# Kernel optimization log

Measured on AMD Instinct MI355X. Metric: run time of the kernel, lower is better.

Reference implementation:

```python
import jax, jax.numpy as jnp
import numpy as np

N_EMBD = 768
N_HEAD = 12
HEAD_DIM = N_EMBD // N_HEAD  # 64


def setup_inputs() -> dict:
    key = jax.random.key(0)
    k1, k2, k3 = jax.random.split(key, 3)
    B, S = 4, 2048
    x = jax.random.normal(k1, (B, S, N_EMBD), dtype=jnp.float32)
    W_attn = jax.random.normal(k2, (N_EMBD, 3 * N_EMBD), dtype=jnp.float32) * 0.02
    b_attn = jax.random.normal(k3, (3 * N_EMBD,), dtype=jnp.float32) * 0.02
    return {"x": x, "W_attn": W_attn, "b_attn": b_attn}


def reference(x, W_attn, b_attn):
    B, S, E = x.shape
    H, D = N_HEAD, HEAD_DIM
    # fused QKV projection (torch Linear: x @ W^T + b; here W_attn stored as [E, 3E])
    qkv = x @ W_attn + b_attn  # [B, S, 3E]
    q, k, v = jnp.split(qkv, 3, axis=-1)
    q = q.reshape(B, S, H, D)
    k = k.reshape(B, S, H, D)
    v = v.reshape(B, S, H, D)
    scale = 1.0 / np.sqrt(D).astype(np.float32)
    scores = jnp.einsum('bqhd,bkhd->bhqk', q, k) * scale  # [B, H, S, S]
    causal = jnp.tril(jnp.ones((S, S), dtype=bool))
    # ReLU attention nonlinearity (no softmax); masked entries -> 0
    att = jnp.where(causal, jnp.maximum(scores, 0.0), 0.0)
    y = jnp.einsum('bhqk,bkhd->bqhd', att, v)  # [B, S, H, D]
    return y.reshape(B, S, E)
```

## Files before the change

### kernel.cpp

```cpp
#include <hip/hip_runtime.h>

typedef __attribute__((ext_vector_type(8))) short short8;
typedef __attribute__((ext_vector_type(4))) float floatx4;
typedef __attribute__((ext_vector_type(4))) unsigned int uint4v;

#define S_LEN 2048
#define NH 12
#define HD 64
#define EMB 768
#define E3 2304

__device__ __forceinline__ unsigned short f2bf(float f) {
    unsigned int u = __builtin_bit_cast(unsigned int, f);
    u += 0x7FFFu + ((u >> 16) & 1u);
    return (unsigned short)(u >> 16);
}

__device__ __forceinline__ unsigned int pack2bf(float a, float b) {
#if __has_builtin(__builtin_amdgcn_cvt_pk_bf16_f32)
    typedef __attribute__((ext_vector_type(2))) short short2v;
    short2v r = __builtin_amdgcn_cvt_pk_bf16_f32(a, b);
    return __builtin_bit_cast(unsigned int, r);
#else
    return (unsigned int)f2bf(a) | ((unsigned int)f2bf(b) << 16);
#endif
}

__device__ __forceinline__ void pl32_swap(unsigned int& x, unsigned int& y) {
#if __has_builtin(__builtin_amdgcn_permlane32_swap)
    typedef __attribute__((ext_vector_type(2))) unsigned int uint2v_;
    uint2v_ r = __builtin_amdgcn_permlane32_swap(x, y, false, false);
    x = r[0]; y = r[1];
#else
    asm("v_permlane32_swap_b32 %0, %1" : "+v"(x), "+v"(y));
#endif
}
__device__ __forceinline__ void pl16_swap(unsigned int& x, unsigned int& y) {
#if __has_builtin(__builtin_amdgcn_permlane16_swap)
    typedef __attribute__((ext_vector_type(2))) unsigned int uint2v_;
    uint2v_ r = __builtin_amdgcn_permlane16_swap(x, y, false, false);
    x = r[0]; y = r[1];
#else
    asm("v_permlane16_swap_b32 %0, %1" : "+v"(x), "+v"(y));
#endif
}

__device__ __forceinline__ void gl_lds16(const void* g, void* l) {
    __builtin_amdgcn_global_load_lds(
        (const __attribute__((address_space(1))) unsigned int*)g,
        (__attribute__((address_space(3))) unsigned int*)l, 16, 0, 0);
}

__global__ __launch_bounds__(256) void conv_fused(const float* __restrict__ x,
                                                  ushort* __restrict__ xb,
                                                  const float* __restrict__ W,
                                                  ushort* __restrict__ Wt) {
    int tid = threadIdx.x;
    if (blockIdx.x < 6144) {
        int i = (blockIdx.x * 256 + tid) * 4;
        float4 f = *(const float4*)(x + i);
        ushort4 o;
        o.x = f2bf(f.x); o.y = f2bf(f.y); o.z = f2bf(f.z); o.w = f2bf(f.w);
        *(ushort4*)(xb + i) = o;
    } else {
        __shared__ float tile[32][33];
        int b2 = blockIdx.x - 6144;
        int n0 = (b2 % 72) * 32, k0 = (b2 / 72) * 32;
        int tx = tid & 31, ty = tid >> 5;
        for (int i = 0; i < 4; i++)
            tile[ty + i * 8][tx] = W[(size_t)(k0 + ty + i * 8) * E3 + n0 + tx];
        __syncthreads();
        for (int i = 0; i < 4; i++)
            Wt[(size_t)(n0 + ty + i * 8) * EMB + k0 + tx] = f2bf(tile[tx][ty + i * 8]);
    }
}

__global__ __launch_bounds__(256) void qkv_gemm(const ushort* __restrict__ Xb,
                                                const ushort* __restrict__ Wt,
                                                const float* __restrict__ bias,
                                                ushort* __restrict__ QKb,
                                                ushort* __restrict__ Vt) {
    __shared__ ushort lds[16896];
    char* ldsb = (char*)lds;
    int tid  = threadIdx.x;
    int wv = tid >> 6, lane = tid & 63;
    int l15 = lane & 15, quad = lane >> 4;
    int r8 = lane >> 3, cc = lane & 7;
    int wm = wv >> 1, wn = wv & 1;
    int m0 = blockIdx.x * 128, n0 = blockIdx.y * 128;

    floatx4 acc[4][4] = {};

    const char* ag = (const char*)(Xb + (size_t)m0 * EMB)
                   + (wv * 32 + r8) * 1536 + (cc ^ r8) * 16;
    const char* bgp = (const char*)(Wt + (size_t)n0 * EMB)
                   + (wv * 32 + r8) * 1536 + (cc ^ r8) * 16;
    int ast = (wv * 32) * 128;
    int bst = 16384 + (wv * 32) * 128;
    int afo[2], bfo[2];
    for (int ch = 0; ch < 2; ch++) {
        int sw = ((ch * 4 + quad) ^ (l15 & 7)) * 16;
        afo[ch] = wm * 8192 + l15 * 128 + sw;
        bfo[ch] = 16384 + wn * 8192 + l15 * 128 + sw;
    }

    for (int k0 = 0; k0 < 12; k0++) {
        __syncthreads();
        for (int i = 0; i < 4; i++) {
            gl_lds16(ag + i * 12288, ldsb + ast + i * 1024);
            gl_lds16(bgp + i * 12288, ldsb + bst + i * 1024);
        }
        ag += 128;  bgp += 128;
        __syncthreads();
        for (int ch = 0; ch < 2; ch++) {
            short8 af[4], bf[4];
            for (int mi = 0; mi < 4; mi++)
                af[mi] = *(const short8*)(ldsb + afo[ch] + mi * 2048);
            for (int ni = 0; ni < 4; ni++)
                bf[ni] = *(const short8*)(ldsb + bfo[ch] + ni * 2048);
            for (int mi = 0; mi < 4; mi++)
                for (int ni = 0; ni < 4; ni++)
                    acc[mi][ni] = __builtin_amdgcn_mfma_f32_16x16x32_bf16(
                        af[mi], bf[ni], acc[mi][ni], 0, 0, 0);
        }
    }

    __syncthreads();
    int seg = n0 / EMB;
    if (seg < 2) {
        float scale = (seg == 0) ? 0.125f : 1.0f;
        for (int ni = 0; ni < 4; ni++) {
            int nl = wn * 64 + ni * 16 + l15;
            float bv = bias[n0 + nl];
            for (int mi = 0; mi < 4; mi++)
                for (int r = 0; r < 4; r++) {
                    int ml = wm * 64 + mi * 16 + quad * 4 + r;
                    lds[ml * 132 + nl] = f2bf((acc[mi][ni][r] + bv) * scale);
                }
        }
        __syncthreads();
        int row = tid >> 1, half2 = tid & 1;
        size_t gm = (size_t)(m0 + row);
        for (int i = 0; i < 8; i++) {
            uint4 v = *(const uint4*)&lds[row * 132 + half2 * 64 + i * 8];
            *(uint4*)&QKb[gm * 1536 + n0 + half2 * 64 + i * 8] = v;
        }
    } else {
        for (int ni = 0; ni < 4; ni++) {
            int nl = wn * 64 + ni * 16 + l15;
            float bv = bias[n0 + nl];
            for (int mi = 0; mi < 4; mi++) {
                int ml = wm * 64 + mi * 16 + quad * 4;
                ushort4 p4;
                p4.x = f2bf(acc[mi][ni][0] + bv);
                p4.y = f2bf(acc[mi][ni][1] + bv);
                p4.z = f2bf(acc[mi][ni][2] + bv);
                p4.w = f2bf(acc[mi][ni][3] + bv);
                *(ushort4*)&lds[nl * 132 + ml] = p4;
            }
        }
        __syncthreads();
        int row = tid >> 1, half2 = tid & 1;
        int nn = n0 + row - 1536;
        int hh = nn >> 6, d = nn & 63;
        int bb = m0 >> 11, s0 = m0 & 2047;
        for (int i = 0; i < 8; i++) {
            uint4 v = *(const uint4*)&lds[row * 132 + half2 * 64 + i * 8];
            *(uint4*)&Vt[((size_t)(bb * NH + hh) * HD + d) * S_LEN + s0 + half2 * 64 + i * 8] = v;
        }
    }
}

__global__ __launch_bounds__(256) void attn(const ushort* __restrict__ QKb,
                                            const ushort* __restrict__ Vt,
                                            float* __restrict__ out) {
    __shared__ ushort lds[32768];
    char* ldsb = (char*)lds;
    int tid = threadIdx.x;
    int w = tid >> 6, lane = tid & 63;
    int l15 = lane & 15, quad = lane >> 4;
    int r8 = lane >> 3, cc = lane & 7;
    int rr = lane >> 4;

    int kfo[2];
    for (int ch = 0; ch < 2; ch++)
        kfo[ch] = l15 * 128 + ((ch * 4 + quad) ^ (l15 & 7)) * 16;
    int vfo2[4];
    for (int T = 0; T < 4; T++)
        vfo2[T] = 32768 + l15 * 256 + ((T * 4 + quad) ^ l15) * 16;
    int rhs[2] = { w * 32 + l15, w * 32 + 16 + l15 };
    int kgo = (w * 32 + r8) * 3072 + (cc ^ r8) * 16;
    int vgo[4];
    for (int i = 0; i < 4; i++)
        vgo[i] = (w * 16 + i * 4 + rr) * 4096 + (((lane & 15) ^ ((i * 4 + rr) & 15)) * 16);
    int kst = (w * 32) * 128;
    int vst = 32768 + (w * 16) * 256;

    int b = blockIdx.x;
    int nit, qts[2], bhs[2];
    if (b < 240)      { nit = 1; qts[0] = 15 - b / 48; bhs[0] = b % 48; qts[1] = 0; bhs[1] = 0; }
    else if (b < 480) { int j = b - 240; nit = 2; qts[0] = 10 - j / 48; bhs[0] = j % 48;
                        qts[1] = 1 + j / 48; bhs[1] = j % 48; }
    else              { int j = b - 480; nit = 2; qts[0] = 0; bhs[0] = 2 * j;
                        qts[1] = 0; bhs[1] = 2 * j + 1; }

    const char* kg[2]; const char* vg[2];
    for (int i = 0; i < 2; i++) {
        int bh = bhs[i], bg = bh / NH, h = bh % NH;
        kg[i] = (const char*)(QKb + (size_t)bg * S_LEN * 1536 + 768 + h * 64) + kgo;
        vg[i] = (const char*)(Vt + (size_t)bh * HD * S_LEN);
    }

    auto prefetch = [&](const char* kbase, const char* vbase, int dstP) {
        for (int i = 0; i < 4; i++)
            gl_lds16(kbase + i * 24576, ldsb + dstP * 16384 + kst + i * 1024);
        for (int i = 0; i < 4; i++)
            gl_lds16(vbase + vgo[i], ldsb + dstP * 16384 + vst + i * 1024);
    };

    int p = 0;
    prefetch(kg[0], vg[0], 0);
    for (int ii = 0; ii < nit; ii++) {
        int qt = qts[ii];
        int bh = bhs[ii], bg = bh / NH, h = bh % NH;
        const ushort* Qcol = QKb + (size_t)bg * S_LEN * 1536 + h * 64;
        short8 qf[2][2];
        for (int nq = 0; nq < 2; nq++)
            for (int ch = 0; ch < 2; ch++)
                qf[nq][ch] = *(const short8*)(Qcol +
                    (size_t)(qt * 128 + w * 32 + nq * 16 + l15) * 1536 + ch * 32 + quad * 8);

        floatx4 acco[2][4] = {};
        int nst = qt + 1;
        for (int st = 0; st < nst; st++) {
            __syncthreads();
            if (st + 1 < nst)
                prefetch(kg[ii] + (size_t)(st + 1) * 393216, vg[ii] + (st + 1) * 256, p ^ 1);
            else if (ii + 1 < nit)
                prefetch(kg[ii + 1], vg[ii + 1], p ^ 1);

            bool diag = (st == qt);
            const char* kb = ldsb + p * 16384;

            for (int jsub = 0; jsub < 2; jsub++) {
                floatx4 stc[4][2] = {};
                for (int ch = 0; ch < 2; ch++) {
                    short8 kf[4];
                    for (int mk = 0; mk < 4; mk++)
                        kf[mk] = *(const short8*)(kb + kfo[ch] + jsub * 8192 + mk * 2048);
                    for (int mk = 0; mk < 4; mk++)
                        for (int nq = 0; nq < 2; nq++)
                            stc[mk][nq] = __builtin_amdgcn_mfma_f32_16x16x32_bf16(
                                kf[mk], qf[nq][ch], stc[mk][nq], 0, 0, 0);
                }

                unsigned int pk[4][2][2];
                for (int mk = 0; mk < 4; mk++) {
                    for (int nq = 0; nq < 2; nq++) {
                        float e[4];
                        for (int r = 0; r < 4; r++)
                            e[r] = fmaxf(stc[mk][nq][r], 0.0f);
                        if (diag) {
                            int kl = jsub * 64 + mk * 16 + quad * 4;
                            for (int r = 0; r < 4; r++)
                                if (kl + r > rhs[nq]) e[r] = 0.0f;
                        }
                        pk[mk][nq][0] = pack2bf(e[0], e[1]);
                        pk[mk][nq][1] = pack2bf(e[2], e[3]);
                    }
                }

                for (int pr = 0; pr < 2; pr++) {
                    int T = jsub * 2 + pr;
                    short8 vf[4];
                    for (int ni = 0; ni < 4; ni++)
                        vf[ni] = *(const short8*)(kb + vfo2[T] + ni * 4096);
                    for (int mi = 0; mi < 2; mi++) {
                        unsigned int a0 = pk[2 * pr][mi][0], a1 = pk[2 * pr][mi][1];
                        unsigned int b0 = pk[2 * pr + 1][mi][0], b1 = pk[2 * pr + 1][mi][1];
                        pl32_swap(a0, b0);  pl32_swap(a1, b1);
                        pl16_swap(a0, b0);  pl16_swap(a1, b1);
                        short8 af = __builtin_bit_cast(short8, (uint4v){a0, a1, b0, b1});
                        for (int ni = 0; ni < 4; ni++)
                            acco[mi][ni] = __builtin_amdgcn_mfma_f32_16x16x32_bf16(
                                af, vf[ni], acco[mi][ni], 0, 0, 0);
                    }
                }
            }
            p ^= 1;
        }

        for (int mi = 0; mi < 2; mi++) {
            for (int ni = 0; ni < 4; ni++) {
                int d = ni * 16 + l15;
                for (int r = 0; r < 4; r++) {
                    int s = qt * 128 + w * 32 + mi * 16 + quad * 4 + r;
                    out[((size_t)bg * S_LEN + s) * EMB + h * 64 + d] = acco[mi][ni][r];
                }
            }
        }
    }
}

extern "C" void kernel_launch(void* const* d_in, const int* in_sizes, int n_in,
                              void* d_out, int out_size, void* d_ws, size_t ws_size,
                              hipStream_t stream) {
    const float* x    = (const float*)d_in[0];
    const float* W    = (const float*)d_in[1];
    const float* bias = (const float*)d_in[2];
    float* out = (float*)d_out;

    char* ws = (char*)d_ws;
    const size_t SZ_X  = (size_t)8192 * EMB * 2;
    const size_t SZ_W  = (size_t)E3 * EMB * 2;
    const size_t SZ_QK = (size_t)8192 * 1536 * 2;
    ushort* Xb  = (ushort*)(ws);
    ushort* Wt  = (ushort*)(ws + SZ_X);
    ushort* QKb = (ushort*)(ws + SZ_X + SZ_W);
    ushort* Vt  = (ushort*)(ws + SZ_X + SZ_W + SZ_QK);

    conv_fused<<<dim3(6144 + 1728), dim3(256), 0, stream>>>(x, Xb, W, Wt);
    qkv_gemm<<<dim3(64, 18), dim3(256), 0, stream>>>(Xb, Wt, bias, QKb, Vt);
    attn<<<dim3(504), dim3(256), 0, stream>>>(QKb, Vt, out);
}
```

Before: 183.6 us.

## Triple-buffer QKV GEMM with 256x128 tiles and interleaved async loads

The QKV GEMM moves to 512-thread blocks covering 256x128 output tiles, using 144KB of dynamic LDS split into three stages. Global-to-LDS loads for stage t+2 are interleaved between MFMA groups, gated by vmcnt waits and barriers, with setprio raised around the MFMA bursts. This targets the load/compute serialization of the old single-buffer loop, which synced twice per k-step, and raises per-block reuse. In exchange the grid halves to 576 blocks and each CU holds one block because of the LDS footprint, and the epilogue is reworked to transpose V for 256 rows.

```diff
diff --git a/kernel.cpp b/kernel.cpp
--- a/kernel.cpp
+++ b/kernel.cpp
@@ -9,6 +9,8 @@
 #define HD 64
 #define EMB 768
 #define E3 2304
+
+#define MF(a, b, c) __builtin_amdgcn_mfma_f32_16x16x32_bf16(a, b, c, 0, 0, 0)
 
 __device__ __forceinline__ unsigned short f2bf(float f) {
     unsigned int u = __builtin_bit_cast(unsigned int, f);
@@ -75,58 +77,107 @@
     }
 }
 
-__global__ __launch_bounds__(256) void qkv_gemm(const ushort* __restrict__ Xb,
-                                                const ushort* __restrict__ Wt,
-                                                const float* __restrict__ bias,
-                                                ushort* __restrict__ QKb,
-                                                ushort* __restrict__ Vt) {
-    __shared__ ushort lds[16896];
-    char* ldsb = (char*)lds;
-    int tid  = threadIdx.x;
-    int wv = tid >> 6, lane = tid & 63;
-    int l15 = lane & 15, quad = lane >> 4;
-    int r8 = lane >> 3, cc = lane & 7;
-    int wm = wv >> 1, wn = wv & 1;
-    int m0 = blockIdx.x * 128, n0 = blockIdx.y * 128;
+__global__ __launch_bounds__(512, 1) void qkv_gemm(const ushort* __restrict__ Xb,
+                                                   const ushort* __restrict__ Wt,
+                                                   const float* __restrict__ bias,
+                                                   ushort* __restrict__ QKb,
+                                                   ushort* __restrict__ Vt) {
+    extern __shared__ char ldsb[];
+    const int tid  = threadIdx.x;
+    const int w = tid >> 6, lane = tid & 63;
+    const int l15 = lane & 15, quad = lane >> 4;
+    const int r8 = lane >> 3, cc = lane & 7;
+    const int wm = w >> 1, wn = w & 1;
+    const int m0 = blockIdx.x * 256, n0 = blockIdx.y * 128;
 
     floatx4 acc[4][4] = {};
 
-    const char* ag = (const char*)(Xb + (size_t)m0 * EMB)
-                   + (wv * 32 + r8) * 1536 + (cc ^ r8) * 16;
-    const char* bgp = (const char*)(Wt + (size_t)n0 * EMB)
-                   + (wv * 32 + r8) * 1536 + (cc ^ r8) * 16;
-    int ast = (wv * 32) * 128;
-    int bst = 16384 + (wv * 32) * 128;
-    int afo[2], bfo[2];
-    for (int ch = 0; ch < 2; ch++) {
-        int sw = ((ch * 4 + quad) ^ (l15 & 7)) * 16;
-        afo[ch] = wm * 8192 + l15 * 128 + sw;
-        bfo[ch] = 16384 + wn * 8192 + l15 * 128 + sw;
-    }
-
-    for (int k0 = 0; k0 < 12; k0++) {
-        __syncthreads();
-        for (int i = 0; i < 4; i++) {
-            gl_lds16(ag + i * 12288, ldsb + ast + i * 1024);
-            gl_lds16(bgp + i * 12288, ldsb + bst + i * 1024);
-        }
-        ag += 128;  bgp += 128;
-        __syncthreads();
-        for (int ch = 0; ch < 2; ch++) {
-            short8 af[4], bf[4];
-            for (int mi = 0; mi < 4; mi++)
-                af[mi] = *(const short8*)(ldsb + afo[ch] + mi * 2048);
-            for (int ni = 0; ni < 4; ni++)
-                bf[ni] = *(const short8*)(ldsb + bfo[ch] + ni * 2048);
-            for (int mi = 0; mi < 4; mi++)
-                for (int ni = 0; ni < 4; ni++)
-                    acc[mi][ni] = __builtin_amdgcn_mfma_f32_16x16x32_bf16(
-                        af[mi], bf[ni], acc[mi][ni], 0, 0, 0);
-        }
+    const char* agp = (const char*)Xb + (size_t)(m0 + w * 32 + r8) * 1536 + (cc ^ r8) * 16;
+    const char* bgp = (const char*)Wt + (size_t)(n0 + w * 16 + r8) * 1536 + (cc ^ r8) * 16;
+    const int adstB = w * 4096;
+    const int bdstB = 32768 + w * 2048;
+
+    const int aroB = (wm * 64 + l15) * 128;
+    const int broB = 32768 + (wn * 64 + l15) * 128;
+    const int swz0 = ((quad) ^ (l15 & 7)) * 16;
+    const int swz1 = ((4 + quad) ^ (l15 & 7)) * 16;
+
+    for (int i = 0; i < 4; i++) gl_lds16(agp + i * 12288, ldsb + adstB + i * 1024);
+    for (int i = 0; i < 2; i++) gl_lds16(bgp + i * 12288, ldsb + bdstB + i * 1024);
+    for (int i = 0; i < 4; i++) gl_lds16(agp + 128 + i * 12288, ldsb + 49152 + adstB + i * 1024);
+    for (int i = 0; i < 2; i++) gl_lds16(bgp + 128 + i * 12288, ldsb + 49152 + bdstB + i * 1024);
+
+#pragma unroll
+    for (int t = 0; t < 12; ++t) {
+        if (t < 11) asm volatile("s_waitcnt vmcnt(6)" ::: "memory");
+        else        asm volatile("s_waitcnt vmcnt(0)" ::: "memory");
+        __builtin_amdgcn_s_barrier();
+        __builtin_amdgcn_sched_barrier(0);
+
+        const char* base = ldsb + (t % 3) * 49152;
+        char* sdst = ldsb + ((t + 2) % 3) * 49152;
+        const int koff = (t + 2) * 128;
+        const bool st = (t < 10);
+
+        short8 af0, af1, bf0, bf1, bf2, bf3;
+
+        af0 = *(const short8*)(base + aroB + 0 * 2048 + swz0);
+        af1 = *(const short8*)(base + aroB + 1 * 2048 + swz0);
+        bf0 = *(const short8*)(base + broB + 0 * 2048 + swz0);
+        bf1 = *(const short8*)(base + broB + 1 * 2048 + swz0);
+        bf2 = *(const short8*)(base + broB + 2 * 2048 + swz0);
+        bf3 = *(const short8*)(base + broB + 3 * 2048 + swz0);
+        if (st) { gl_lds16(agp + koff,         sdst + adstB);
+                  gl_lds16(agp + koff + 12288, sdst + adstB + 1024); }
+        __builtin_amdgcn_s_setprio(1);
+        acc[0][0] = MF(af0, bf0, acc[0][0]); acc[0][1] = MF(af0, bf1, acc[0][1]);
+        acc[0][2] = MF(af0, bf2, acc[0][2]); acc[0][3] = MF(af0, bf3, acc[0][3]);
+        acc[1][0] = MF(af1, bf0, acc[1][0]); acc[1][1] = MF(af1, bf1, acc[1][1]);
+        acc[1][2] = MF(af1, bf2, acc[1][2]); acc[1][3] = MF(af1, bf3, acc[1][3]);
+        __builtin_amdgcn_s_setprio(0);
+        __builtin_amdgcn_s_barrier();
+
+        af0 = *(const short8*)(base + aroB + 2 * 2048 + swz0);
+        af1 = *(const short8*)(base + aroB + 3 * 2048 + swz0);
+        if (st) { gl_lds16(agp + koff + 2 * 12288, sdst + adstB + 2048);
+                  gl_lds16(agp + koff + 3 * 12288, sdst + adstB + 3072); }
+        __builtin_amdgcn_s_setprio(1);
+        acc[2][0] = MF(af0, bf0, acc[2][0]); acc[2][1] = MF(af0, bf1, acc[2][1]);
+        acc[2][2] = MF(af0, bf2, acc[2][2]); acc[2][3] = MF(af0, bf3, acc[2][3]);
+        acc[3][0] = MF(af1, bf0, acc[3][0]); acc[3][1] = MF(af1, bf1, acc[3][1]);
+        acc[3][2] = MF(af1, bf2, acc[3][2]); acc[3][3] = MF(af1, bf3, acc[3][3]);
+        __builtin_amdgcn_s_setprio(0);
+        __builtin_amdgcn_s_barrier();
+
+        af0 = *(const short8*)(base + aroB + 0 * 2048 + swz1);
+        af1 = *(const short8*)(base + aroB + 1 * 2048 + swz1);
+        bf0 = *(const short8*)(base + broB + 0 * 2048 + swz1);
+        bf1 = *(const short8*)(base + broB + 1 * 2048 + swz1);
+        bf2 = *(const short8*)(base + broB + 2 * 2048 + swz1);
+        bf3 = *(const short8*)(base + broB + 3 * 2048 + swz1);
+        if (st) { gl_lds16(bgp + koff,         sdst + bdstB);
+                  gl_lds16(bgp + koff + 12288, sdst + bdstB + 1024); }
+        __builtin_amdgcn_s_setprio(1);
+        acc[0][0] = MF(af0, bf0, acc[0][0]); acc[0][1] = MF(af0, bf1, acc[0][1]);
+        acc[0][2] = MF(af0, bf2, acc[0][2]); acc[0][3] = MF(af0, bf3, acc[0][3]);
+        acc[1][0] = MF(af1, bf0, acc[1][0]); acc[1][1] = MF(af1, bf1, acc[1][1]);
+        acc[1][2] = MF(af1, bf2, acc[1][2]); acc[1][3] = MF(af1, bf3, acc[1][3]);
+        __builtin_amdgcn_s_setprio(0);
+        __builtin_amdgcn_s_barrier();
+
+        af0 = *(const short8*)(base + aroB + 2 * 2048 + swz1);
+        af1 = *(const short8*)(base + aroB + 3 * 2048 + swz1);
+        __builtin_amdgcn_s_setprio(1);
+        acc[2][0] = MF(af0, bf0, acc[2][0]); acc[2][1] = MF(af0, bf1, acc[2][1]);
+        acc[2][2] = MF(af0, bf2, acc[2][2]); acc[2][3] = MF(af0, bf3, acc[2][3]);
+        acc[3][0] = MF(af1, bf0, acc[3][0]); acc[3][1] = MF(af1, bf1, acc[3][1]);
+        acc[3][2] = MF(af1, bf2, acc[3][2]); acc[3][3] = MF(af1, bf3, acc[3][3]);
+        __builtin_amdgcn_s_setprio(0);
     }
 
     __syncthreads();
-    int seg = n0 / EMB;
+    ushort* epi = (ushort*)ldsb;
+    int seg = n0 >= 1536 ? 2 : (n0 >= 768 ? 1 : 0);
     if (seg < 2) {
         float scale = (seg == 0) ? 0.125f : 1.0f;
         for (int ni = 0; ni < 4; ni++) {
@@ -135,15 +186,15 @@
             for (int mi = 0; mi < 4; mi++)
                 for (int r = 0; r < 4; r++) {
                     int ml = wm * 64 + mi * 16 + quad * 4 + r;
-                    lds[ml * 132 + nl] = f2bf((acc[mi][ni][r] + bv) * scale);
+                    epi[ml * 132 + nl] = f2bf((acc[mi][ni][r] + bv) * scale);
                 }
         }
         __syncthreads();
-        int row = tid >> 1, half2 = tid & 1;
+        int row = tid >> 1, h2 = tid & 1;
         size_t gm = (size_t)(m0 + row);
         for (int i = 0; i < 8; i++) {
-            uint4 v = *(const uint4*)&lds[row * 132 + half2 * 64 + i * 8];
-            *(uint4*)&QKb[gm * 1536 + n0 + half2 * 64 + i * 8] = v;
+            uint4 v = *(const uint4*)&epi[row * 132 + h2 * 64 + i * 8];
+            *(uint4*)&QKb[gm * 1536 + n0 + h2 * 64 + i * 8] = v;
         }
     } else {
         for (int ni = 0; ni < 4; ni++) {
@@ -156,17 +207,17 @@
                 p4.y = f2bf(acc[mi][ni][1] + bv);
                 p4.z = f2bf(acc[mi][ni][2] + bv);
                 p4.w = f2bf(acc[mi][ni][3] + bv);
-                *(ushort4*)&lds[nl * 132 + ml] = p4;
+                *(ushort4*)&epi[nl * 264 + ml] = p4;
             }
         }
         __syncthreads();
-        int row = tid >> 1, half2 = tid & 1;
+        int row = tid >> 2, q4 = tid & 3;
         int nn = n0 + row - 1536;
         int hh = nn >> 6, d = nn & 63;
         int bb = m0 >> 11, s0 = m0 & 2047;
         for (int i = 0; i < 8; i++) {
-            uint4 v = *(const uint4*)&lds[row * 132 + half2 * 64 + i * 8];
-            *(uint4*)&Vt[((size_t)(bb * NH + hh) * HD + d) * S_LEN + s0 + half2 * 64 + i * 8] = v;
+            uint4 v = *(const uint4*)&epi[row * 264 + q4 * 64 + i * 8];
+            *(uint4*)&Vt[((size_t)(bb * NH + hh) * HD + d) * S_LEN + s0 + q4 * 64 + i * 8] = v;
         }
     }
 }
@@ -319,7 +370,14 @@
     ushort* QKb = (ushort*)(ws + SZ_X + SZ_W);
     ushort* Vt  = (ushort*)(ws + SZ_X + SZ_W + SZ_QK);
 
+    static bool attr_done = false;
+    if (!attr_done) {
+        hipFuncSetAttribute((const void*)qkv_gemm,
+                            hipFuncAttributeMaxDynamicSharedMemorySize, 147456);
+        attr_done = true;
+    }
+
     conv_fused<<<dim3(6144 + 1728), dim3(256), 0, stream>>>(x, Xb, W, Wt);
-    qkv_gemm<<<dim3(64, 18), dim3(256), 0, stream>>>(Xb, Wt, bias, QKb, Vt);
+    qkv_gemm<<<dim3(32, 18), dim3(512), 147456, stream>>>(Xb, Wt, bias, QKb, Vt);
     attn<<<dim3(504), dim3(256), 0, stream>>>(QKb, Vt, out);
 }
```

After: 186.5 us. About the same (+1.6%).
